# Performance work log

Measured on AMD Instinct MI355X. Metric: run time of the kernel, lower is better.

## Reference

```python
import jax, jax.numpy as jnp
import numpy as np

N = 50000          # nodes
E = 1000000        # edges
EMB = 64           # emb_dim
L = 3              # num_layer
B = 250            # graphs (200 nodes each)
XF, EF = 7, 5      # node / edge feature dims
BN_EPS = 1e-5


def setup_inputs() -> dict:
    key = jax.random.key(0)
    ks = jax.random.split(key, 16)
    x = jax.random.normal(ks[0], (N, XF), dtype=jnp.float32)
    edge_attr = jax.random.normal(ks[1], (E, EF), dtype=jnp.float32)
    edge_index = jax.random.randint(ks[2], (2, E), 0, N, dtype=jnp.int32)
    # 250 contiguous graphs of 200 nodes: last node index of each graph
    last_idx = jnp.arange(1, B + 1, dtype=jnp.int32) * (N // B) - 1
    s = 0.05
    xW = jax.random.normal(ks[3], (XF, EMB), dtype=jnp.float32) * s
    xb = jnp.zeros((EMB,), dtype=jnp.float32)
    eW = jax.random.normal(ks[4], (L, EF, EMB), dtype=jnp.float32) * s
    eb = jnp.zeros((L, EMB), dtype=jnp.float32)
    W1 = jax.random.normal(ks[5], (L, EMB, 2 * EMB), dtype=jnp.float32) * s
    b1 = jnp.zeros((L, 2 * EMB), dtype=jnp.float32)
    W2 = jax.random.normal(ks[6], (L, 2 * EMB, EMB), dtype=jnp.float32) * s
    b2 = jnp.zeros((L, EMB), dtype=jnp.float32)
    gamma = jnp.ones((L, EMB), dtype=jnp.float32)
    beta = jnp.zeros((L, EMB), dtype=jnp.float32)
    return {"x": x, "edge_attr": edge_attr, "edge_index": edge_index,
            "last_idx": last_idx, "xW": xW, "xb": xb, "eW": eW, "eb": eb,
            "W1": W1, "b1": b1, "W2": W2, "b2": b2,
            "gamma": gamma, "beta": beta}


def _gnn_forward(x, edge_attr, edge_index, last_idx, xW, xb, eW, eb, W1, b1, W2, b2, gamma, beta):
    n = x.shape[0]
    # self-loop edge attrs: first column = 8, rest 0
    self_attr = jnp.zeros((n, EF), dtype=edge_attr.dtype).at[:, 0].set(8.0)
    ea = jnp.concatenate([edge_attr, self_attr], axis=0)          # [E+N, EF]
    loop = jnp.arange(n, dtype=edge_index.dtype)
    src = jnp.concatenate([edge_index[0], loop])                  # x_j indices
    dst = jnp.concatenate([edge_index[1], loop])                  # aggregation targets

    h = x @ xW + xb                                               # [N, EMB]
    for l in range(L):
        e = ea @ eW[l] + eb[l]                                    # [E+N, EMB]
        msg = h[src] + e                                          # gather + combine
        agg = jax.ops.segment_sum(msg, dst, num_segments=n)       # scatter-add
        h2 = jax.nn.relu(agg @ W1[l] + b1[l]) @ W2[l] + b2[l]     # GIN MLP
        mean = jnp.mean(h2, axis=0)
        var = jnp.mean(jnp.square(h2 - mean), axis=0)             # biased, like torch BN
        hn = (h2 - mean) * jax.lax.rsqrt(var + BN_EPS) * gamma[l] + beta[l]
        h = jax.nn.elu(hn) if l < L - 1 else hn                   # drop_ratio = 0
    return h[last_idx]                                            # super-node reps [B, EMB]


def reference(x, edge_attr, edge_index, last_idx, xW, xb, eW, eb, W1, b1, W2, b2, gamma, beta):
    return _gnn_forward(x, edge_attr, edge_index, last_idx, xW, xb, eW, eb, W1, b1, W2, b2, gamma, beta)
```

## Files before the change

### kernel.cpp

```cpp
#include <hip/hip_runtime.h>

#define N_NODES 50000
#define N_EDGES 1000000
#define EMB     64
#define HID     128
#define NLAYER  3
#define NGRAPH  250
#define XFD     7
#define EFD     5
#define BN_EPS  1e-5f

#define BKT_SH 8
#define BKT_SZ 256
#define NBKT   ((N_NODES + BKT_SZ - 1) / BKT_SZ)
#define CHKE   4096
#define NCHK   ((N_EDGES + CHKE - 1) / CHKE)
#define CNTM   (NBKT * NCHK)
#define NB2    ((CNTM + 255) / 256)

typedef short bf8_t __attribute__((ext_vector_type(8)));
typedef float f4_t  __attribute__((ext_vector_type(4)));

union FragU {
    uint4 q;
    bf8_t v;
    unsigned short u[8];
};

__device__ __forceinline__ void atomAddF(float* p, float v) {
    __hip_atomic_fetch_add(p, v, __ATOMIC_RELAXED, __HIP_MEMORY_SCOPE_AGENT);
}

__device__ __forceinline__ unsigned short f2bf(float f) {
    unsigned int u = __float_as_uint(f);
    u += 0x7fffu + ((u >> 16) & 1u);
    return (unsigned short)(u >> 16);
}
__device__ __forceinline__ float bf2f(unsigned short s) {
    return __uint_as_float(((unsigned int)s) << 16);
}
__device__ __forceinline__ float4 bf4(ushort4 u) {
    return make_float4(bf2f(u.x), bf2f(u.y), bf2f(u.z), bf2f(u.w));
}

__global__ void k_input(const float* __restrict__ x, const float* __restrict__ xW,
                        const float* __restrict__ xb, unsigned short* __restrict__ h) {
    int gid = blockIdx.x * 256 + threadIdx.x;
    if (gid >= N_NODES * EMB) return;
    int n = gid >> 6, f = gid & 63;
    float acc = xb[f];
#pragma unroll
    for (int k = 0; k < XFD; ++k) acc = fmaf(x[n * XFD + k], xW[k * EMB + f], acc);
    h[gid] = f2bf(acc);
}

__global__ void k_packW(const float* __restrict__ W1, const float* __restrict__ W2,
                        unsigned short* __restrict__ pw1, unsigned short* __restrict__ pw2) {
    int gid = blockIdx.x * 256 + threadIdx.x;
    int layer = gid >> 14;
    int r = gid & 16383;
    if (layer >= NLAYER) return;
    if (r < 8192) {
        int p = r;
        int j = p & 7, lane = (p >> 3) & 63, ts = p >> 9;
        int t = ts >> 1, s = ts & 1;
        int k = 32 * s + 8 * (lane >> 4) + j;
        int n = 16 * t + (lane & 15);
        pw1[layer * 8192 + p] = f2bf(W1[layer * EMB * HID + k * HID + n]);
    } else {
        int p = r - 8192;
        int j = p & 7, lane = (p >> 3) & 63, ts = p >> 9;
        int t = ts >> 2, s = ts & 3;
        int k = 32 * s + 8 * (lane >> 4) + j;
        int n = 16 * t + (lane & 15);
        pw2[layer * 8192 + p] = f2bf(W2[layer * HID * EMB + k * EMB + n]);
    }
}

__global__ __launch_bounds__(256) void k_binA(const int* __restrict__ dst,
                                              int* __restrict__ cntmat) {
    __shared__ int hist[NBKT];
    int tid = threadIdx.x, c = blockIdx.x;
    for (int i = tid; i < NBKT; i += 256) hist[i] = 0;
    __syncthreads();
    int e0 = c * CHKE, e1 = min(e0 + CHKE, N_EDGES);
    for (int i = e0 + tid; i < e1; i += 256) atomicAdd(&hist[dst[i] >> BKT_SH], 1);
    __syncthreads();
    for (int b = tid; b < NBKT; b += 256) cntmat[b * NCHK + c] = hist[b];
}

__global__ __launch_bounds__(256) void k_gscanA(const int* __restrict__ in, int n,
                                                int* __restrict__ bsum) {
    int tid = threadIdx.x, lane = tid & 63, wid = tid >> 6;
    int i = blockIdx.x * 256 + tid;
    int v = (i < n) ? in[i] : 0;
#pragma unroll
    for (int off = 32; off; off >>= 1) v += __shfl_down(v, off);
    __shared__ int ws[4];
    if (lane == 0) ws[wid] = v;
    __syncthreads();
    if (tid == 0) bsum[blockIdx.x] = ws[0] + ws[1] + ws[2] + ws[3];
}

__global__ __launch_bounds__(256) void k_gscanB(const int* __restrict__ bsum, int nb,
                                                int* __restrict__ boff) {
    int tid = threadIdx.x, lane = tid & 63, wid = tid >> 6;
    int v = (tid < nb) ? bsum[tid] : 0;
    int x = v;
#pragma unroll
    for (int off = 1; off < 64; off <<= 1) {
        int y = __shfl_up(x, off);
        if (lane >= off) x += y;
    }
    __shared__ int wtot[4];
    if (lane == 63) wtot[wid] = x;
    __syncthreads();
    int woff = 0;
    for (int w = 0; w < wid; ++w) woff += wtot[w];
    if (tid < nb) boff[tid] = woff + x - v;
}

__global__ __launch_bounds__(256) void k_gscanC(const int* __restrict__ in, int n,
                                                const int* __restrict__ boff,
                                                int* __restrict__ out) {
    int tid = threadIdx.x, lane = tid & 63, wid = tid >> 6;
    int i = blockIdx.x * 256 + tid;
    int v = (i < n) ? in[i] : 0;
    int x = v;
#pragma unroll
    for (int off = 1; off < 64; off <<= 1) {
        int y = __shfl_up(x, off);
        if (lane >= off) x += y;
    }
    __shared__ int wtot[4];
    if (lane == 63) wtot[wid] = x;
    __syncthreads();
    int woff = boff[blockIdx.x];
    for (int w = 0; w < wid; ++w) woff += wtot[w];
    if (i < n) out[i] = woff + x - v;
}

__global__ __launch_bounds__(256) void k_binC(const int* __restrict__ src,
                                              const int* __restrict__ dst,
                                              const int* __restrict__ off2,
                                              int2* __restrict__ bufSD) {
    __shared__ int cur[NBKT];
    int tid = threadIdx.x, c = blockIdx.x;
    for (int b = tid; b < NBKT; b += 256) cur[b] = off2[b * NCHK + c];
    __syncthreads();
    int e0 = c * CHKE, e1 = min(e0 + CHKE, N_EDGES);
    for (int i = e0 + tid; i < e1; i += 256) {
        int d = dst[i];
        int b = d >> BKT_SH;
        int p = atomicAdd(&cur[b], 1);
        bufSD[p] = make_int2(src[i], ((d & (BKT_SZ - 1)) << 20) | i);
    }
}

__global__ __launch_bounds__(256) void k_binD(const int2* __restrict__ bufSD,
                                              const int* __restrict__ off2,
                                              int* __restrict__ csr,
                                              int* __restrict__ csrE,
                                              int* __restrict__ rowstart) {
    __shared__ int hist[BKT_SZ];
    __shared__ int cur[BKT_SZ];
    __shared__ int wtot[4];
    int tid = threadIdx.x, b = blockIdx.x;
    int bstart = off2[b * NCHK];
    int bend = (b + 1 < NBKT) ? off2[(b + 1) * NCHK] : N_EDGES;
    hist[tid] = 0;
    __syncthreads();
    for (int j = bstart + tid; j < bend; j += 256)
        atomicAdd(&hist[bufSD[j].y >> 20], 1);
    __syncthreads();
    int lane = tid & 63, wid = tid >> 6;
    int v = hist[tid], x = v;
#pragma unroll
    for (int off = 1; off < 64; off <<= 1) {
        int y = __shfl_up(x, off);
        if (lane >= off) x += y;
    }
    if (lane == 63) wtot[wid] = x;
    __syncthreads();
    int woff = 0;
    for (int w = 0; w < wid; ++w) woff += wtot[w];
    int ex = woff + x - v;
    cur[tid] = ex;
    int node = b * BKT_SZ + tid;
    if (node < N_NODES) rowstart[node] = bstart + ex;
    if (b == NBKT - 1 && tid == 0) rowstart[N_NODES] = N_EDGES;
    __syncthreads();
    for (int j = bstart + tid; j < bend; j += 256) {
        int2 t = bufSD[j];
        int local = t.y >> 20;
        int p = atomicAdd(&cur[local], 1);
        csr[bstart + p] = t.x;
        csrE[bstart + p] = t.y & 0xFFFFF;
    }
}

__global__ __launch_bounds__(256) void k_aggE(const int* __restrict__ rowstart,
                                              const int* __restrict__ csrE,
                                              const float* __restrict__ ea,
                                              float* __restrict__ aggE) {
    int wid = (blockIdx.x * 256 + threadIdx.x) >> 6;
    int lane = threadIdx.x & 63;
    if (wid >= N_NODES) return;
    int j0 = rowstart[wid], j1 = rowstart[wid + 1];
    float s0 = 0.f, s1 = 0.f, s2 = 0.f, s3 = 0.f, s4 = 0.f;
    for (int j = j0 + lane; j < j1; j += 64) {
        int e = csrE[j];
        const float* p = ea + (size_t)e * EFD;
        s0 += p[0]; s1 += p[1]; s2 += p[2]; s3 += p[3]; s4 += p[4];
    }
#pragma unroll
    for (int off = 32; off; off >>= 1) {
        s0 += __shfl_down(s0, off);
        s1 += __shfl_down(s1, off);
        s2 += __shfl_down(s2, off);
        s3 += __shfl_down(s3, off);
        s4 += __shfl_down(s4, off);
    }
    if (lane == 0) {
        float* o = aggE + (size_t)wid * EFD;
        o[0] = s0; o[1] = s1; o[2] = s2; o[3] = s3; o[4] = s4;
    }
}

#define ACC4(acc, u) { float4 _v = bf4(u); acc.x += _v.x; acc.y += _v.y; acc.z += _v.z; acc.w += _v.w; }

__global__ __launch_bounds__(256) void k_agg(const unsigned short* __restrict__ h,
                                             unsigned short* __restrict__ aggb,
                                             const int* __restrict__ rowstart,
                                             const int* __restrict__ csr,
                                             const float* __restrict__ aggE,
                                             const float* __restrict__ eWl,
                                             const float* __restrict__ ebl) {
    int wave = (blockIdx.x * 256 + threadIdx.x) >> 6;
    int lane = threadIdx.x & 63;
    int nbase = wave * 4;
    if (nbase >= N_NODES) return;
    int lg = lane >> 4, lq = lane & 15;
    const ushort4* hb = (const ushort4*)h;
    const float4* eW4 = (const float4*)eWl;
    float4 ew0 = eW4[lq], ew1 = eW4[16 + lq], ew2 = eW4[32 + lq],
           ew3 = eW4[48 + lq], ew4 = eW4[64 + lq];
    float4 eb4 = ((const float4*)ebl)[lq];
#pragma unroll
    for (int half = 0; half < 2; ++half) {
        int nA = nbase + half * 2;
        int nB = nA + 1;
        int rA0 = rowstart[nA], rA1 = rowstart[nA + 1], rB1 = rowstart[nB + 1];
        int jA = rA0, jB = rA1;
        float4 accA = make_float4(0.f, 0.f, 0.f, 0.f);
        float4 accB = make_float4(0.f, 0.f, 0.f, 0.f);
        while (jA < rA1 || jB < rB1) {
            int takeA = min(rA1 - jA, 64); if (takeA < 0) takeA = 0;
            int takeB = min(rB1 - jB, 64); if (takeB < 0) takeB = 0;
            int myA = (lane < takeA) ? csr[jA + lane] : 0;
            int myB = (lane < takeB) ? csr[jB + lane] : 0;
            int nt = (max(takeA, takeB) + 3) >> 2;
            int t = 0;
            for (; t + 4 <= nt; t += 4) {
                int e0 = t * 4 + lg, e1 = e0 + 4, e2 = e0 + 8, e3 = e0 + 12;
                int sA0 = __shfl(myA, e0), sA1 = __shfl(myA, e1),
                    sA2 = __shfl(myA, e2), sA3 = __shfl(myA, e3);
                int sB0 = __shfl(myB, e0), sB1 = __shfl(myB, e1),
                    sB2 = __shfl(myB, e2), sB3 = __shfl(myB, e3);
                ushort4 uA0 = hb[(size_t)sA0 * 16 + lq];
                ushort4 uA1 = hb[(size_t)sA1 * 16 + lq];
                ushort4 uA2 = hb[(size_t)sA2 * 16 + lq];
                ushort4 uA3 = hb[(size_t)sA3 * 16 + lq];
                ushort4 uB0 = hb[(size_t)sB0 * 16 + lq];
                ushort4 uB1 = hb[(size_t)sB1 * 16 + lq];
                ushort4 uB2 = hb[(size_t)sB2 * 16 + lq];
                ushort4 uB3 = hb[(size_t)sB3 * 16 + lq];
                if (e0 < takeA) ACC4(accA, uA0);
                if (e1 < takeA) ACC4(accA, uA1);
                if (e2 < takeA) ACC4(accA, uA2);
                if (e3 < takeA) ACC4(accA, uA3);
                if (e0 < takeB) ACC4(accB, uB0);
                if (e1 < takeB) ACC4(accB, uB1);
                if (e2 < takeB) ACC4(accB, uB2);
                if (e3 < takeB) ACC4(accB, uB3);
            }
            for (; t < nt; ++t) {
                int e = t * 4 + lg;
                int sA = __shfl(myA, e), sB = __shfl(myB, e);
                ushort4 uA = hb[(size_t)sA * 16 + lq];
                ushort4 uB = hb[(size_t)sB * 16 + lq];
                if (e < takeA) ACC4(accA, uA);
                if (e < takeB) ACC4(accB, uB);
            }
            jA += takeA;
            jB += takeB;
        }
        accA.x += __shfl_xor(accA.x, 16); accA.y += __shfl_xor(accA.y, 16);
        accA.z += __shfl_xor(accA.z, 16); accA.w += __shfl_xor(accA.w, 16);
        accA.x += __shfl_xor(accA.x, 32); accA.y += __shfl_xor(accA.y, 32);
        accA.z += __shfl_xor(accA.z, 32); accA.w += __shfl_xor(accA.w, 32);
        accB.x += __shfl_xor(accB.x, 16); accB.y += __shfl_xor(accB.y, 16);
        accB.z += __shfl_xor(accB.z, 16); accB.w += __shfl_xor(accB.w, 16);
        accB.x += __shfl_xor(accB.x, 32); accB.y += __shfl_xor(accB.y, 32);
        accB.x += 0.f;
        accB.z += __shfl_xor(accB.z, 32); accB.w += __shfl_xor(accB.w, 32);
#pragma unroll
        for (int pick = 0; pick < 2; ++pick) {
            int n = pick ? nB : nA;
            float4 acc = pick ? accB : accA;
            int deg = (pick ? (rB1 - rA1) : (rA1 - rA0));
            float a0 = aggE[n * 5 + 0], a1 = aggE[n * 5 + 1], a2 = aggE[n * 5 + 2],
                  a3 = aggE[n * 5 + 3], a4 = aggE[n * 5 + 4];
            float c0 = a0 + 8.f;
            float ce = (float)deg + 1.f;
            float4 bb = bf4(hb[(size_t)n * 16 + lq]);
            bb.x = fmaf(c0, ew0.x, bb.x); bb.y = fmaf(c0, ew0.y, bb.y);
            bb.z = fmaf(c0, ew0.z, bb.z); bb.w = fmaf(c0, ew0.w, bb.w);
            bb.x = fmaf(a1, ew1.x, bb.x); bb.y = fmaf(a1, ew1.y, bb.y);
            bb.z = fmaf(a1, ew1.z, bb.z); bb.w = fmaf(a1, ew1.w, bb.w);
            bb.x = fmaf(a2, ew2.x, bb.x); bb.y = fmaf(a2, ew2.y, bb.y);
            bb.z = fmaf(a2, ew2.z, bb.z); bb.w = fmaf(a2, ew2.w, bb.w);
            bb.x = fmaf(a3, ew3.x, bb.x); bb.y = fmaf(a3, ew3.y, bb.y);
            bb.z = fmaf(a3, ew3.z, bb.z); bb.w = fmaf(a3, ew3.w, bb.w);
            bb.x = fmaf(a4, ew4.x, bb.x); bb.y = fmaf(a4, ew4.y, bb.y);
            bb.z = fmaf(a4, ew4.z, bb.z); bb.w = fmaf(a4, ew4.w, bb.w);
            bb.x = fmaf(ce, eb4.x, bb.x); bb.y = fmaf(ce, eb4.y, bb.y);
            bb.z = fmaf(ce, eb4.z, bb.z); bb.w = fmaf(ce, eb4.w, bb.w);
            if (lg == 0) {
                ushort4 o;
                o.x = f2bf(acc.x + bb.x);
                o.y = f2bf(acc.y + bb.y);
                o.z = f2bf(acc.z + bb.z);
                o.w = f2bf(acc.w + bb.w);
                ((ushort4*)aggb)[(size_t)n * 16 + lq] = o;
            }
        }
    }
}

__global__ __launch_bounds__(256) void k_mlp(const unsigned short* __restrict__ aggb,
                                             float* __restrict__ h2,
                                             const unsigned short* __restrict__ pw1,
                                             const float* __restrict__ b1l,
                                             const unsigned short* __restrict__ pw2,
                                             const float* __restrict__ b2l,
                                             float* __restrict__ stats) {
    __shared__ __align__(16) unsigned short hid[64 * 136];
    int tid = threadIdx.x;
    int w = tid >> 6, lane = tid & 63;
    int q = lane >> 4, l15 = lane & 15;
    int n0 = blockIdx.x * 64;
    int mrow = n0 + 16 * w + l15;
    const unsigned short* arow =
        aggb + (size_t)(mrow < N_NODES ? mrow : N_NODES - 1) * EMB;
    FragU fa[2];
    fa[0].q = *(const uint4*)&arow[8 * q];
    fa[1].q = *(const uint4*)&arow[32 + 8 * q];
    const uint4* w1f = (const uint4*)pw1;
    f4_t acc1[8];
#pragma unroll
    for (int t = 0; t < 8; ++t) {
        acc1[t] = (f4_t){0.f, 0.f, 0.f, 0.f};
        FragU b0, b1;
        b0.q = w1f[(t * 2 + 0) * 64 + lane];
        b1.q = w1f[(t * 2 + 1) * 64 + lane];
        acc1[t] = __builtin_amdgcn_mfma_f32_16x16x32_bf16(fa[0].v, b0.v, acc1[t], 0, 0, 0);
        acc1[t] = __builtin_amdgcn_mfma_f32_16x16x32_bf16(fa[1].v, b1.v, acc1[t], 0, 0, 0);
    }
#pragma unroll
    for (int t = 0; t < 8; ++t) {
        int col = 16 * t + l15;
        float bv = b1l[col];
#pragma unroll
        for (int r = 0; r < 4; ++r) {
            int m = 16 * w + q * 4 + r;
            hid[m * 136 + col] = f2bf(fmaxf(acc1[t][r] + bv, 0.f));
        }
    }
    FragU fa2[4];
#pragma unroll
    for (int s = 0; s < 4; ++s)
        fa2[s].q = *(const uint4*)&hid[(16 * w + l15) * 136 + 32 * s + 8 * q];
    const uint4* w2f = (const uint4*)pw2;
    f4_t acc2[4];
#pragma unroll
    for (int t = 0; t < 4; ++t) {
        acc2[t] = (f4_t){0.f, 0.f, 0.f, 0.f};
#pragma unroll
        for (int s = 0; s < 4; ++s) {
            FragU b;
            b.q = w2f[(t * 4 + s) * 64 + lane];
            acc2[t] = __builtin_amdgcn_mfma_f32_16x16x32_bf16(fa2[s].v, b.v, acc2[t], 0, 0, 0);
        }
    }
    float sacc[4] = {0.f, 0.f, 0.f, 0.f}, qacc[4] = {0.f, 0.f, 0.f, 0.f};
#pragma unroll
    for (int t = 0; t < 4; ++t) {
        int col = 16 * t + l15;
        float bv = b2l[col];
#pragma unroll
        for (int r = 0; r < 4; ++r) {
            int nn = n0 + 16 * w + q * 4 + r;
            if (nn < N_NODES) {
                float v = acc2[t][r] + bv;
                h2[(size_t)nn * EMB + col] = v;
                sacc[t] += v;
                qacc[t] = fmaf(v, v, qacc[t]);
            }
        }
    }
#pragma unroll
    for (int t = 0; t < 4; ++t) {
        sacc[t] += __shfl_xor(sacc[t], 16); qacc[t] += __shfl_xor(qacc[t], 16);
        sacc[t] += __shfl_xor(sacc[t], 32); qacc[t] += __shfl_xor(qacc[t], 32);
    }
    __syncthreads();
    float* red = (float*)hid;
    if (q == 0) {
#pragma unroll
        for (int t = 0; t < 4; ++t) {
            red[w * 64 + 16 * t + l15] = sacc[t];
            red[256 + w * 64 + 16 * t + l15] = qacc[t];
        }
    }
    __syncthreads();
    if (tid < 64) {
        float s = red[tid] + red[64 + tid] + red[128 + tid] + red[192 + tid];
        float qq = red[256 + tid] + red[320 + tid] + red[384 + tid] + red[448 + tid];
        atomAddF(&stats[tid], s);
        atomAddF(&stats[64 + tid], qq);
    }
}

__global__ void k_bn(const float* __restrict__ h2, unsigned short* __restrict__ h,
                     const float* __restrict__ stats, const float* __restrict__ gam,
                     const float* __restrict__ bet) {
    int gid = blockIdx.x * 256 + threadIdx.x;
    if (gid >= N_NODES * EMB) return;
    int f = gid & 63;
    const float invN = 1.f / (float)N_NODES;
    float mean = stats[f] * invN;
    float var = stats[64 + f] * invN - mean * mean;
    float inv = rsqrtf(var + BN_EPS);
    float v = (h2[gid] - mean) * inv * gam[f] + bet[f];
    h[gid] = f2bf(v > 0.f ? v : expm1f(v));
}

__global__ void k_bnout(const float* __restrict__ h2, const int* __restrict__ last,
                        const float* __restrict__ stats, const float* __restrict__ gam,
                        const float* __restrict__ bet, float* __restrict__ out) {
    int gid = blockIdx.x * 256 + threadIdx.x;
    if (gid >= NGRAPH * EMB) return;
    int b = gid >> 6, f = gid & 63;
    const float invN = 1.f / (float)N_NODES;
    float mean = stats[f] * invN;
    float var = stats[64 + f] * invN - mean * mean;
    float inv = rsqrtf(var + BN_EPS);
    out[gid] = (h2[last[b] * EMB + f] - mean) * inv * gam[f] + bet[f];
}

extern "C" void kernel_launch(void* const* d_in, const int* in_sizes, int n_in,
                              void* d_out, int out_size, void* d_ws, size_t ws_size,
                              hipStream_t stream) {
    const float* x   = (const float*)d_in[0];
    const float* ea  = (const float*)d_in[1];
    const int*   eidx= (const int*)d_in[2];
    const int*   last= (const int*)d_in[3];
    const float* xW  = (const float*)d_in[4];
    const float* xb  = (const float*)d_in[5];
    const float* eW  = (const float*)d_in[6];
    const float* eb  = (const float*)d_in[7];
    const float* W1  = (const float*)d_in[8];
    const float* b1  = (const float*)d_in[9];
    const float* W2  = (const float*)d_in[10];
    const float* b2  = (const float*)d_in[11];
    const float* gam = (const float*)d_in[12];
    const float* bet = (const float*)d_in[13];
    float* out = (float*)d_out;

    const int* srcI = eidx;
    const int* dstI = eidx + N_EDGES;

    float* hslot  = (float*)d_ws;
    float* agg    = hslot + N_NODES * EMB;
    float* hidslot= agg + N_NODES * EMB;
    float* aggE   = hidslot + N_NODES * HID;
    float* stats  = aggE + NBKT * BKT_SZ * EFD;
    int* rowstart = (int*)(stats + NLAYER * 2 * EMB);
    int* csr      = rowstart + N_NODES + 1;
    int* cntmat   = csr + N_EDGES;
    int* off2     = cntmat + CNTM;
    int* bsum     = off2 + CNTM;
    int* boff     = bsum + NB2;
    unsigned short* pw1 = (unsigned short*)(boff + NB2);
    unsigned short* pw2 = pw1 + NLAYER * EMB * HID;
    unsigned short* h = (unsigned short*)hslot;
    unsigned short* aggb = (unsigned short*)hidslot;
    int2* bufSD   = (int2*)agg;
    int*  csrE    = (int*)hidslot;

    hipMemsetAsync(stats, 0, NLAYER * 2 * EMB * sizeof(float), stream);

    k_input<<<(N_NODES * EMB + 255) / 256, 256, 0, stream>>>(x, xW, xb, h);
    k_packW<<<(NLAYER * 2 * EMB * HID + 255) / 256, 256, 0, stream>>>(W1, W2, pw1, pw2);
    k_binA<<<NCHK, 256, 0, stream>>>(dstI, cntmat);
    k_gscanA<<<NB2, 256, 0, stream>>>(cntmat, CNTM, bsum);
    k_gscanB<<<1, 256, 0, stream>>>(bsum, NB2, boff);
    k_gscanC<<<NB2, 256, 0, stream>>>(cntmat, CNTM, boff, off2);
    k_binC<<<NCHK, 256, 0, stream>>>(srcI, dstI, off2, bufSD);
    k_binD<<<NBKT, 256, 0, stream>>>(bufSD, off2, csr, csrE, rowstart);
    k_aggE<<<(N_NODES * 64 + 255) / 256, 256, 0, stream>>>(rowstart, csrE, ea, aggE);

    const int aggBlocks = ((N_NODES + 3) / 4 * 64 + 255) / 256;
    const int mlpBlocks = (N_NODES + 63) / 64;
    for (int l = 0; l < NLAYER; ++l) {
        k_agg<<<aggBlocks, 256, 0, stream>>>(
            h, aggb, rowstart, csr, aggE, eW + l * EFD * EMB, eb + l * EMB);
        k_mlp<<<mlpBlocks, 256, 0, stream>>>(aggb, agg, pw1 + l * EMB * HID, b1 + l * HID,
                                             pw2 + l * HID * EMB, b2 + l * EMB,
                                             stats + l * 2 * EMB);
        if (l < NLAYER - 1) {
            k_bn<<<(N_NODES * EMB + 255) / 256, 256, 0, stream>>>(
                agg, h, stats + l * 2 * EMB, gam + l * EMB, bet + l * EMB);
        } else {
            k_bnout<<<(NGRAPH * EMB + 255) / 256, 256, 0, stream>>>(
                agg, last, stats + l * 2 * EMB, gam + l * EMB, bet + l * EMB, out);
        }
    }
}
```

Before: 347.2 us.

## Fuse per-layer agg/MLP/BN kernels into one cooperative persistent kernel

Replaces the nine per-layer kernel launches (aggregate, MLP, batchnorm for each of three layers) with a single cooperative kernel of 512 blocks that loops over layers and separates the stages with grid-wide syncs. The goal is to remove launch overhead and inter-kernel gaps. The cost is that a fixed-size persistent grid may give lower occupancy and worse load balance for the gather stage, and each grid barrier adds its own latency. If the cooperative launch fails, the code falls back to the old multi-kernel path.

```diff
diff --git a/kernel.cpp b/kernel.cpp
--- a/kernel.cpp
+++ b/kernel.cpp
@@ -1,4 +1,7 @@
 #include <hip/hip_runtime.h>
+#include <hip/hip_cooperative_groups.h>
+
+namespace cg = cooperative_groups;
 
 #define N_NODES 50000
 #define N_EDGES 1000000
@@ -9,6 +12,7 @@
 #define XFD     7
 #define EFD     5
 #define BN_EPS  1e-5f
+#define COOP_GRID 512
 
 #define BKT_SH 8
 #define BKT_SZ 256
@@ -229,23 +233,11 @@
 
 #define ACC4(acc, u) { float4 _v = bf4(u); acc.x += _v.x; acc.y += _v.y; acc.z += _v.z; acc.w += _v.w; }
 
-__global__ __launch_bounds__(256) void k_agg(const unsigned short* __restrict__ h,
-                                             unsigned short* __restrict__ aggb,
-                                             const int* __restrict__ rowstart,
-                                             const int* __restrict__ csr,
-                                             const float* __restrict__ aggE,
-                                             const float* __restrict__ eWl,
-                                             const float* __restrict__ ebl) {
-    int wave = (blockIdx.x * 256 + threadIdx.x) >> 6;
-    int lane = threadIdx.x & 63;
-    int nbase = wave * 4;
-    if (nbase >= N_NODES) return;
-    int lg = lane >> 4, lq = lane & 15;
-    const ushort4* hb = (const ushort4*)h;
-    const float4* eW4 = (const float4*)eWl;
-    float4 ew0 = eW4[lq], ew1 = eW4[16 + lq], ew2 = eW4[32 + lq],
-           ew3 = eW4[48 + lq], ew4 = eW4[64 + lq];
-    float4 eb4 = ((const float4*)ebl)[lq];
+__device__ __forceinline__ void agg_waveunit(
+    int nbase, int lane, int lg, int lq,
+    const ushort4* hb, const int* __restrict__ rowstart, const int* __restrict__ csr,
+    const float* __restrict__ aggE, float4 ew0, float4 ew1, float4 ew2, float4 ew3,
+    float4 ew4, float4 eb4, unsigned short* __restrict__ aggb) {
 #pragma unroll
     for (int half = 0; half < 2; ++half) {
         int nA = nbase + half * 2;
@@ -302,7 +294,6 @@
         accB.x += __shfl_xor(accB.x, 16); accB.y += __shfl_xor(accB.y, 16);
         accB.z += __shfl_xor(accB.z, 16); accB.w += __shfl_xor(accB.w, 16);
         accB.x += __shfl_xor(accB.x, 32); accB.y += __shfl_xor(accB.y, 32);
-        accB.x += 0.f;
         accB.z += __shfl_xor(accB.z, 32); accB.w += __shfl_xor(accB.w, 32);
 #pragma unroll
         for (int pick = 0; pick < 2; ++pick) {
@@ -338,6 +329,183 @@
     }
 }
 
+__device__ __forceinline__ void mlp_tile(
+    int n0, int tid, int w, int lane, int q, int l15,
+    const unsigned short* __restrict__ aggb, float* __restrict__ h2,
+    const unsigned short* __restrict__ pw1l, const float* __restrict__ b1l,
+    const unsigned short* __restrict__ pw2l, const float* __restrict__ b2l,
+    float* __restrict__ statsl, unsigned short* hid) {
+    int mrow = n0 + 16 * w + l15;
+    const unsigned short* arow =
+        aggb + (size_t)(mrow < N_NODES ? mrow : N_NODES - 1) * EMB;
+    FragU fa[2];
+    fa[0].q = *(const uint4*)&arow[8 * q];
+    fa[1].q = *(const uint4*)&arow[32 + 8 * q];
+    const uint4* w1f = (const uint4*)pw1l;
+    f4_t acc1[8];
+#pragma unroll
+    for (int t = 0; t < 8; ++t) {
+        acc1[t] = (f4_t){0.f, 0.f, 0.f, 0.f};
+        FragU b0, bq1;
+        b0.q = w1f[(t * 2 + 0) * 64 + lane];
+        bq1.q = w1f[(t * 2 + 1) * 64 + lane];
+        acc1[t] = __builtin_amdgcn_mfma_f32_16x16x32_bf16(fa[0].v, b0.v, acc1[t], 0, 0, 0);
+        acc1[t] = __builtin_amdgcn_mfma_f32_16x16x32_bf16(fa[1].v, bq1.v, acc1[t], 0, 0, 0);
+    }
+#pragma unroll
+    for (int t = 0; t < 8; ++t) {
+        int col = 16 * t + l15;
+        float bv = b1l[col];
+#pragma unroll
+        for (int r = 0; r < 4; ++r) {
+            int m = 16 * w + q * 4 + r;
+            hid[m * 136 + col] = f2bf(fmaxf(acc1[t][r] + bv, 0.f));
+        }
+    }
+    FragU fa2[4];
+#pragma unroll
+    for (int s = 0; s < 4; ++s)
+        fa2[s].q = *(const uint4*)&hid[(16 * w + l15) * 136 + 32 * s + 8 * q];
+    const uint4* w2f = (const uint4*)pw2l;
+    f4_t acc2[4];
+#pragma unroll
+    for (int t = 0; t < 4; ++t) {
+        acc2[t] = (f4_t){0.f, 0.f, 0.f, 0.f};
+#pragma unroll
+        for (int s = 0; s < 4; ++s) {
+            FragU b;
+            b.q = w2f[(t * 4 + s) * 64 + lane];
+            acc2[t] = __builtin_amdgcn_mfma_f32_16x16x32_bf16(fa2[s].v, b.v, acc2[t], 0, 0, 0);
+        }
+    }
+    float sacc[4] = {0.f, 0.f, 0.f, 0.f}, qacc[4] = {0.f, 0.f, 0.f, 0.f};
+#pragma unroll
+    for (int t = 0; t < 4; ++t) {
+        int col = 16 * t + l15;
+        float bv = b2l[col];
+#pragma unroll
+        for (int r = 0; r < 4; ++r) {
+            int nn = n0 + 16 * w + q * 4 + r;
+            if (nn < N_NODES) {
+                float v = acc2[t][r] + bv;
+                h2[(size_t)nn * EMB + col] = v;
+                sacc[t] += v;
+                qacc[t] = fmaf(v, v, qacc[t]);
+            }
+        }
+    }
+#pragma unroll
+    for (int t = 0; t < 4; ++t) {
+        sacc[t] += __shfl_xor(sacc[t], 16); qacc[t] += __shfl_xor(qacc[t], 16);
+        sacc[t] += __shfl_xor(sacc[t], 32); qacc[t] += __shfl_xor(qacc[t], 32);
+    }
+    __syncthreads();
+    float* red = (float*)hid;
+    if (q == 0) {
+#pragma unroll
+        for (int t = 0; t < 4; ++t) {
+            red[w * 64 + 16 * t + l15] = sacc[t];
+            red[256 + w * 64 + 16 * t + l15] = qacc[t];
+        }
+    }
+    __syncthreads();
+    if (tid < 64) {
+        float s = red[tid] + red[64 + tid] + red[128 + tid] + red[192 + tid];
+        float qq = red[256 + tid] + red[320 + tid] + red[384 + tid] + red[448 + tid];
+        atomAddF(&statsl[tid], s);
+        atomAddF(&statsl[64 + tid], qq);
+    }
+    __syncthreads();
+}
+
+__global__ __launch_bounds__(256, 4) void k_layers(
+    const int* __restrict__ rowstart, const int* __restrict__ csr,
+    const float* __restrict__ aggE, unsigned short* __restrict__ h,
+    unsigned short* __restrict__ aggb, float* __restrict__ h2,
+    const float* __restrict__ eW, const float* __restrict__ eb,
+    const unsigned short* __restrict__ pw1, const float* __restrict__ b1,
+    const unsigned short* __restrict__ pw2, const float* __restrict__ b2,
+    const float* __restrict__ gam, const float* __restrict__ bet,
+    float* __restrict__ stats, const int* __restrict__ last,
+    float* __restrict__ out) {
+    cg::grid_group gridg = cg::this_grid();
+    __shared__ __align__(16) unsigned short hid[64 * 136];
+    int tid = threadIdx.x;
+    int lane = tid & 63;
+    int lg = lane >> 4, lq = lane & 15;
+    int w = tid >> 6;
+    int q = lane >> 4, l15 = lane & 15;
+
+    for (int l = 0; l < NLAYER; ++l) {
+        {
+            const float4* eW4 = (const float4*)(eW + l * EFD * EMB);
+            float4 ew0 = eW4[lq], ew1 = eW4[16 + lq], ew2 = eW4[32 + lq],
+                   ew3 = eW4[48 + lq], ew4 = eW4[64 + lq];
+            float4 eb4 = ((const float4*)(eb + l * EMB))[lq];
+            const ushort4* hb = (const ushort4*)h;
+            int wslot = blockIdx.x * 4 + w;
+            int gridWaves = gridDim.x * 4;
+            for (int wv = wslot; wv < N_NODES / 4; wv += gridWaves)
+                agg_waveunit(wv * 4, lane, lg, lq, hb, rowstart, csr, aggE,
+                             ew0, ew1, ew2, ew3, ew4, eb4, aggb);
+        }
+        gridg.sync();
+        {
+            const int ntile = (N_NODES + 63) / 64;
+            for (int tile = blockIdx.x; tile < ntile; tile += gridDim.x)
+                mlp_tile(tile * 64, tid, w, lane, q, l15, aggb, h2,
+                         pw1 + l * EMB * HID, b1 + l * HID, pw2 + l * HID * EMB,
+                         b2 + l * EMB, stats + l * 2 * EMB, hid);
+        }
+        gridg.sync();
+        const float* statsl = stats + l * 2 * EMB;
+        const float* gaml = gam + l * EMB;
+        const float* betl = bet + l * EMB;
+        const float invN = 1.f / (float)N_NODES;
+        if (l < NLAYER - 1) {
+            for (int gid = blockIdx.x * 256 + tid; gid < N_NODES * EMB;
+                 gid += gridDim.x * 256) {
+                int f = gid & 63;
+                float mean = statsl[f] * invN;
+                float var = statsl[64 + f] * invN - mean * mean;
+                float inv = rsqrtf(var + BN_EPS);
+                float v = (h2[gid] - mean) * inv * gaml[f] + betl[f];
+                h[gid] = f2bf(v > 0.f ? v : expm1f(v));
+            }
+            gridg.sync();
+        } else {
+            for (int gid = blockIdx.x * 256 + tid; gid < NGRAPH * EMB;
+                 gid += gridDim.x * 256) {
+                int b = gid >> 6, f = gid & 63;
+                float mean = statsl[f] * invN;
+                float var = statsl[64 + f] * invN - mean * mean;
+                float inv = rsqrtf(var + BN_EPS);
+                out[gid] = (h2[(size_t)last[b] * EMB + f] - mean) * inv * gaml[f] + betl[f];
+            }
+        }
+    }
+}
+
+__global__ __launch_bounds__(256) void k_agg(const unsigned short* __restrict__ h,
+                                             unsigned short* __restrict__ aggb,
+                                             const int* __restrict__ rowstart,
+                                             const int* __restrict__ csr,
+                                             const float* __restrict__ aggE,
+                                             const float* __restrict__ eWl,
+                                             const float* __restrict__ ebl) {
+    int wave = (blockIdx.x * 256 + threadIdx.x) >> 6;
+    int lane = threadIdx.x & 63;
+    int nbase = wave * 4;
+    if (nbase >= N_NODES) return;
+    int lg = lane >> 4, lq = lane & 15;
+    const float4* eW4 = (const float4*)eWl;
+    float4 ew0 = eW4[lq], ew1 = eW4[16 + lq], ew2 = eW4[32 + lq],
+           ew3 = eW4[48 + lq], ew4 = eW4[64 + lq];
+    float4 eb4 = ((const float4*)ebl)[lq];
+    agg_waveunit(nbase, lane, lg, lq, (const ushort4*)h, rowstart, csr, aggE,
+                 ew0, ew1, ew2, ew3, ew4, eb4, aggb);
+}
+
 __global__ __launch_bounds__(256) void k_mlp(const unsigned short* __restrict__ aggb,
                                              float* __restrict__ h2,
                                              const unsigned short* __restrict__ pw1,
@@ -349,87 +517,8 @@
     int tid = threadIdx.x;
     int w = tid >> 6, lane = tid & 63;
     int q = lane >> 4, l15 = lane & 15;
-    int n0 = blockIdx.x * 64;
-    int mrow = n0 + 16 * w + l15;
-    const unsigned short* arow =
-        aggb + (size_t)(mrow < N_NODES ? mrow : N_NODES - 1) * EMB;
-    FragU fa[2];
-    fa[0].q = *(const uint4*)&arow[8 * q];
-    fa[1].q = *(const uint4*)&arow[32 + 8 * q];
-    const uint4* w1f = (const uint4*)pw1;
-    f4_t acc1[8];
-#pragma unroll
-    for (int t = 0; t < 8; ++t) {
-        acc1[t] = (f4_t){0.f, 0.f, 0.f, 0.f};
-        FragU b0, b1;
-        b0.q = w1f[(t * 2 + 0) * 64 + lane];
-        b1.q = w1f[(t * 2 + 1) * 64 + lane];
-        acc1[t] = __builtin_amdgcn_mfma_f32_16x16x32_bf16(fa[0].v, b0.v, acc1[t], 0, 0, 0);
-        acc1[t] = __builtin_amdgcn_mfma_f32_16x16x32_bf16(fa[1].v, b1.v, acc1[t], 0, 0, 0);
-    }
-#pragma unroll
-    for (int t = 0; t < 8; ++t) {
-        int col = 16 * t + l15;
-        float bv = b1l[col];
-#pragma unroll
-        for (int r = 0; r < 4; ++r) {
-            int m = 16 * w + q * 4 + r;
-            hid[m * 136 + col] = f2bf(fmaxf(acc1[t][r] + bv, 0.f));
-        }
-    }
-    FragU fa2[4];
-#pragma unroll
-    for (int s = 0; s < 4; ++s)
-        fa2[s].q = *(const uint4*)&hid[(16 * w + l15) * 136 + 32 * s + 8 * q];
-    const uint4* w2f = (const uint4*)pw2;
-    f4_t acc2[4];
-#pragma unroll
-    for (int t = 0; t < 4; ++t) {
-        acc2[t] = (f4_t){0.f, 0.f, 0.f, 0.f};
-#pragma unroll
-        for (int s = 0; s < 4; ++s) {
-            FragU b;
-            b.q = w2f[(t * 4 + s) * 64 + lane];
-            acc2[t] = __builtin_amdgcn_mfma_f32_16x16x32_bf16(fa2[s].v, b.v, acc2[t], 0, 0, 0);
-        }
-    }
-    float sacc[4] = {0.f, 0.f, 0.f, 0.f}, qacc[4] = {0.f, 0.f, 0.f, 0.f};
-#pragma unroll
-    for (int t = 0; t < 4; ++t) {
-        int col = 16 * t + l15;
-        float bv = b2l[col];
-#pragma unroll
-        for (int r = 0; r < 4; ++r) {
-            int nn = n0 + 16 * w + q * 4 + r;
-            if (nn < N_NODES) {
-                float v = acc2[t][r] + bv;
-                h2[(size_t)nn * EMB + col] = v;
-                sacc[t] += v;
-                qacc[t] = fmaf(v, v, qacc[t]);
-            }
-        }
-    }
-#pragma unroll
-    for (int t = 0; t < 4; ++t) {
-        sacc[t] += __shfl_xor(sacc[t], 16); qacc[t] += __shfl_xor(qacc[t], 16);
-        sacc[t] += __shfl_xor(sacc[t], 32); qacc[t] += __shfl_xor(qacc[t], 32);
-    }
-    __syncthreads();
-    float* red = (float*)hid;
-    if (q == 0) {
-#pragma unroll
-        for (int t = 0; t < 4; ++t) {
-            red[w * 64 + 16 * t + l15] = sacc[t];
-            red[256 + w * 64 + 16 * t + l15] = qacc[t];
-        }
-    }
-    __syncthreads();
-    if (tid < 64) {
-        float s = red[tid] + red[64 + tid] + red[128 + tid] + red[192 + tid];
-        float qq = red[256 + tid] + red[320 + tid] + red[384 + tid] + red[448 + tid];
-        atomAddF(&stats[tid], s);
-        atomAddF(&stats[64 + tid], qq);
-    }
+    mlp_tile(blockIdx.x * 64, tid, w, lane, q, l15, aggb, h2, pw1, b1l, pw2, b2l,
+             stats, hid);
 }
 
 __global__ void k_bn(const float* __restrict__ h2, unsigned short* __restrict__ h,
@@ -498,6 +587,7 @@
     unsigned short* aggb = (unsigned short*)hidslot;
     int2* bufSD   = (int2*)agg;
     int*  csrE    = (int*)hidslot;
+    float* h2     = agg;
 
     hipMemsetAsync(stats, 0, NLAYER * 2 * EMB * sizeof(float), stream);
 
@@ -511,20 +601,29 @@
     k_binD<<<NBKT, 256, 0, stream>>>(bufSD, off2, csr, csrE, rowstart);
     k_aggE<<<(N_NODES * 64 + 255) / 256, 256, 0, stream>>>(rowstart, csrE, ea, aggE);
 
-    const int aggBlocks = ((N_NODES + 3) / 4 * 64 + 255) / 256;
-    const int mlpBlocks = (N_NODES + 63) / 64;
-    for (int l = 0; l < NLAYER; ++l) {
-        k_agg<<<aggBlocks, 256, 0, stream>>>(
-            h, aggb, rowstart, csr, aggE, eW + l * EFD * EMB, eb + l * EMB);
-        k_mlp<<<mlpBlocks, 256, 0, stream>>>(aggb, agg, pw1 + l * EMB * HID, b1 + l * HID,
-                                             pw2 + l * HID * EMB, b2 + l * EMB,
-                                             stats + l * 2 * EMB);
-        if (l < NLAYER - 1) {
-            k_bn<<<(N_NODES * EMB + 255) / 256, 256, 0, stream>>>(
-                agg, h, stats + l * 2 * EMB, gam + l * EMB, bet + l * EMB);
-        } else {
-            k_bnout<<<(NGRAPH * EMB + 255) / 256, 256, 0, stream>>>(
-                agg, last, stats + l * 2 * EMB, gam + l * EMB, bet + l * EMB, out);
-        }
-    }
-}
+    void* args[] = {(void*)&rowstart, (void*)&csr, (void*)&aggE, (void*)&h,
+                    (void*)&aggb, (void*)&h2, (void*)&eW, (void*)&eb,
+                    (void*)&pw1, (void*)&b1, (void*)&pw2, (void*)&b2,
+                    (void*)&gam, (void*)&bet, (void*)&stats, (void*)&last,
+                    (void*)&out};
+    hipError_t cerr = hipLaunchCooperativeKernel((void*)k_layers, dim3(COOP_GRID),
+                                                 dim3(256), args, 0, stream);
+    if (cerr != hipSuccess) {
+        const int aggBlocks = ((N_NODES + 3) / 4 * 64 + 255) / 256;
+        const int mlpBlocks = (N_NODES + 63) / 64;
+        for (int l = 0; l < NLAYER; ++l) {
+            k_agg<<<aggBlocks, 256, 0, stream>>>(
+                h, aggb, rowstart, csr, aggE, eW + l * EFD * EMB, eb + l * EMB);
+            k_mlp<<<mlpBlocks, 256, 0, stream>>>(aggb, agg, pw1 + l * EMB * HID,
+                                                 b1 + l * HID, pw2 + l * HID * EMB,
+                                                 b2 + l * EMB, stats + l * 2 * EMB);
+            if (l < NLAYER - 1) {
+                k_bn<<<(N_NODES * EMB + 255) / 256, 256, 0, stream>>>(
+                    agg, h, stats + l * 2 * EMB, gam + l * EMB, bet + l * EMB);
+            } else {
+                k_bnout<<<(NGRAPH * EMB + 255) / 256, 256, 0, stream>>>(
+                    agg, last, stats + l * 2 * EMB, gam + l * EMB, bet + l * EMB, out);
+            }
+        }
+    }
+}
```

After: 893.7 us. 2.57x slower.
